# Kernel tuning notes

Hardware: AMD Instinct MI355X
Metric: run time of the kernel (lower is better)

Reference implementation:

```python
import jax, jax.numpy as jnp
import numpy as np

DIM = 4096
N_HEADS = 32
N_KV_HEADS = 8
HEAD_DIM = DIM // N_HEADS  # 128
KV_DIM = N_KV_HEADS * HEAD_DIM  # 1024
B, T = 2, 1024


def setup_inputs() -> dict:
    key = jax.random.key(0)
    ks = jax.random.split(key, 5)
    s1 = 1.0 / np.sqrt(DIM)
    return {
        "x": jax.random.normal(ks[0], (B, T, DIM), dtype=jnp.float32),
        "W1": jax.random.uniform(ks[1], (DIM + 2 * KV_DIM, DIM), dtype=jnp.float32, minval=-s1, maxval=s1),
        "b1": jax.random.uniform(ks[2], (DIM + 2 * KV_DIM,), dtype=jnp.float32, minval=-s1, maxval=s1),
        "W2": jax.random.uniform(ks[3], (DIM, DIM), dtype=jnp.float32, minval=-s1, maxval=s1),
        "b2": jax.random.uniform(ks[4], (DIM,), dtype=jnp.float32, minval=-s1, maxval=s1),
    }


def reference(x, W1, b1, W2, b2):
    Bn, Tn, D = x.shape
    G = N_HEADS // N_KV_HEADS
    qkv = x @ W1.T + b1  # [B,T,D+2*KV_DIM]
    q = qkv[:, :, :DIM]
    k = qkv[:, :, DIM:DIM + KV_DIM]
    v = qkv[:, :, DIM + KV_DIM:]
    # Faithful to torch repeat_interleave(G, dim=-1): scalar-level interleave on flat feature dim
    k = jnp.repeat(k, G, axis=-1)  # [B,T,D]
    v = jnp.repeat(v, G, axis=-1)
    q = q.reshape(Bn, Tn, N_HEADS, HEAD_DIM).transpose(0, 2, 1, 3)  # [B,H,T,hd]
    k = k.reshape(Bn, Tn, N_HEADS, HEAD_DIM).transpose(0, 2, 1, 3)
    v = v.reshape(Bn, Tn, N_HEADS, HEAD_DIM).transpose(0, 2, 1, 3)
    scale = 1.0 / jnp.sqrt(jnp.asarray(HEAD_DIM, dtype=x.dtype))
    qk = jnp.einsum('bhqd,bhkd->bhqk', q, k) * scale  # [B,H,T,T]
    causal = jnp.tril(jnp.ones((Tn, Tn), dtype=bool))
    qk = jnp.where(causal[None, None], qk, jnp.asarray(-jnp.inf, dtype=qk.dtype))
    att = jax.nn.softmax(qk, axis=-1)
    out = jnp.einsum('bhqk,bhkd->bhqd', att, v)  # [B,H,T,hd]
    out = out.transpose(0, 2, 1, 3).reshape(Bn, Tn, D)
    return out @ W2.T + b2
```

## Files before the change

### kernel.cpp

```cpp
#include <hip/hip_runtime.h>

#define DIMX  4096
#define NH    32
#define HD    128
#define BB    2
#define TT    1024
#define MROWS (BB*TT)
#define CQKV  3072
#define SCALE_Q 0.12751743f

typedef _Float16 half_t;
typedef __attribute__((ext_vector_type(4))) _Float16 f16x4;
typedef __attribute__((ext_vector_type(8))) _Float16 f16x8;
typedef __attribute__((ext_vector_type(4))) float    f32x4;

__device__ __forceinline__ void async_copy16(const void* gsrc, void* ldst) {
  __builtin_amdgcn_global_load_lds(
      (const __attribute__((address_space(1))) unsigned int*)gsrc,
      (__attribute__((address_space(3))) unsigned int*)ldst,
      16, 0, 0);
}

__global__ __launch_bounds__(256) void cvt_f32_f16_kernel(
    const float4* __restrict__ src, f16x4* __restrict__ dst, int n4) {
  int stride = gridDim.x * blockDim.x;
  for (int i = blockIdx.x * blockDim.x + threadIdx.x; i < n4; i += stride) {
    float4 f = src[i];
    f16x4 h;
    h.x = (_Float16)f.x; h.y = (_Float16)f.y;
    h.z = (_Float16)f.z; h.w = (_Float16)f.w;
    dst[i] = h;
  }
}

__global__ __launch_bounds__(256) void fold_w1_kernel(
    const float* __restrict__ W1, const float* __restrict__ b1,
    half_t* __restrict__ W1f, float* __restrict__ b1f)
{
  long idx = (long)blockIdx.x * 256 + threadIdx.x;
  int row = (int)(idx >> 10);
  int c4  = ((int)idx & 1023) << 2;
  f16x4 h;
  if (row < 1024) {
    const float* s = W1 + ((long)row << 2) * DIMX + c4;
    float4 a = *(const float4*)s;
    float4 b = *(const float4*)(s + DIMX);
    float4 c = *(const float4*)(s + 2 * DIMX);
    float4 d = *(const float4*)(s + 3 * DIMX);
    h.x = (_Float16)((a.x + b.x + c.x + d.x) * SCALE_Q);
    h.y = (_Float16)((a.y + b.y + c.y + d.y) * SCALE_Q);
    h.z = (_Float16)((a.z + b.z + c.z + d.z) * SCALE_Q);
    h.w = (_Float16)((a.w + b.w + c.w + d.w) * SCALE_Q);
    if (c4 == 0) {
      const float* bb = b1 + ((long)row << 2);
      b1f[row] = (bb[0] + bb[1] + bb[2] + bb[3]) * SCALE_Q;
    }
  } else {
    const float* s = W1 + ((long)(row + 3072)) * DIMX + c4;
    float4 a = *(const float4*)s;
    h.x = (_Float16)a.x; h.y = (_Float16)a.y;
    h.z = (_Float16)a.z; h.w = (_Float16)a.w;
    if (c4 == 0) b1f[row] = b1[row + 3072];
  }
  *(f16x4*)&W1f[(long)row * DIMX + c4] = h;
}

__global__ __launch_bounds__(256) void fold_w2_kernel(
    const float* __restrict__ W2, half_t* __restrict__ W2f)
{
  long idx = (long)blockIdx.x * 256 + threadIdx.x;
  int row = (int)(idx >> 8);
  int j4  = ((int)idx & 255) << 2;
  const float* s = W2 + (long)row * DIMX + ((long)j4 << 2);
  float4 a = *(const float4*)s;
  float4 b = *(const float4*)(s + 4);
  float4 c = *(const float4*)(s + 8);
  float4 d = *(const float4*)(s + 12);
  f16x4 h;
  h.x = (_Float16)(a.x + a.y + a.z + a.w);
  h.y = (_Float16)(b.x + b.y + b.z + b.w);
  h.z = (_Float16)(c.x + c.y + c.z + c.w);
  h.w = (_Float16)(d.x + d.y + d.z + d.w);
  *(f16x4*)&W2f[(long)row * 1024 + j4] = h;
}

template<int OUT_IS_F16>
__global__ __launch_bounds__(256) void gemm_nt_bias(
    const half_t* __restrict__ A, const half_t* __restrict__ Bw,
    const float* __restrict__ bias, void* __restrict__ Cout,
    int M, int N, int K)
{
  __shared__ alignas(16) half_t As[128 * 32];
  __shared__ alignas(16) half_t Bs[128 * 32];

  const int tid  = threadIdx.x;
  const int lane = tid & 63;
  const int w    = tid >> 6;
  const long row0 = (long)blockIdx.y * 128;
  const long col0 = (long)blockIdx.x * 128;

  const int rr = tid >> 2;
  const int cc = (tid & 3) * 8;
  const half_t* ga0 = A  + (row0 + rr)      * K + cc;
  const half_t* ga1 = A  + (row0 + 64 + rr) * K + cc;
  const half_t* gb0 = Bw + (col0 + rr)      * K + cc;
  const half_t* gb1 = Bw + (col0 + 64 + rr) * K + cc;
  half_t* la0 = &As[w * 512];
  half_t* la1 = &As[2048 + w * 512];
  half_t* lb0 = &Bs[w * 512];
  half_t* lb1 = &Bs[2048 + w * 512];

  const int wm = (w >> 1) * 64;
  const int wn = (w & 1) * 64;
  const int fr = lane & 15;
  const int fk = (lane >> 4) * 8;
  const half_t* pa = &As[(wm + fr) * 32 + fk];
  const half_t* pb = &Bs[(wn + fr) * 32 + fk];

  f32x4 acc[4][4] = {};

  for (int kt = 0; kt < K; kt += 32) {
    __syncthreads();
    async_copy16(ga0 + kt, la0);
    async_copy16(ga1 + kt, la1);
    async_copy16(gb0 + kt, lb0);
    async_copy16(gb1 + kt, lb1);
    __syncthreads();

    f16x8 af[4], bf[4];
#pragma unroll
    for (int mi = 0; mi < 4; ++mi) af[mi] = *(const f16x8*)(pa + mi * 16 * 32);
#pragma unroll
    for (int ni = 0; ni < 4; ++ni) bf[ni] = *(const f16x8*)(pb + ni * 16 * 32);
#pragma unroll
    for (int mi = 0; mi < 4; ++mi)
#pragma unroll
      for (int ni = 0; ni < 4; ++ni)
        acc[mi][ni] = __builtin_amdgcn_mfma_f32_16x16x32_f16(
            af[mi], bf[ni], acc[mi][ni], 0, 0, 0);
  }

  const int er = (lane >> 4) * 4;
  const int ec = lane & 15;
#pragma unroll
  for (int mi = 0; mi < 4; ++mi) {
#pragma unroll
    for (int ni = 0; ni < 4; ++ni) {
      long gn = col0 + wn + ni * 16 + ec;
      float bv = bias[gn];
#pragma unroll
      for (int r = 0; r < 4; ++r) {
        long gm = row0 + wm + mi * 16 + er + r;
        float v = acc[mi][ni][r] + bv;
        if (OUT_IS_F16) ((half_t*)Cout)[gm * N + gn] = (half_t)v;
        else            ((float*)Cout)[gm * N + gn]  = v;
      }
    }
  }
}

#define VTS 72
#define PSS 72
__global__ __launch_bounds__(256, 4) void attn_kernel(
    const half_t* __restrict__ qkv,
    half_t* __restrict__ attc)
{
  __shared__ alignas(16) half_t Ks[64 * 32];
  __shared__ alignas(16) half_t Vt[48 * VTS];
  __shared__ alignas(16) half_t Ps[4][16 * PSS];

  const int tid  = threadIdx.x;
  const int lane = tid & 63;
  const int w    = tid >> 6;
  const int low  = lane & 15;
  const int quad = lane >> 4;
  const int bh   = blockIdx.y;
  const int b    = bh >> 5;
  const int h    = bh & 31;
  const long rb  = (long)b * TT;

  if (tid < 8) {
    f16x8 one;
#pragma unroll
    for (int i = 0; i < 8; ++i) one[i] = (_Float16)1.0f;
    *(f16x8*)&Vt[32 * VTS + tid * 8] = one;
  }

  const int srow = tid >> 2;
  const int sc4  = (tid & 3) << 3;
  half_t* ksdst  = &Ks[w * 512];
  half_t* psw    = &Ps[w][0];
  float*  Ob     = (float*)psw;

  for (int pass = 0; pass < 2; ++pass) {
    const int tile = pass ? (int)blockIdx.x : 15 - (int)blockIdx.x;
    const int t0   = tile * 64;
    const int qg   = t0 + 16 * w;

    f16x8 qf = *(const f16x8*)&qkv[(rb + qg + low) * CQKV + h * 32 + quad * 8];

    f32x4 acc0 = {}, acc1 = {}, acc2 = {};
    const f32x4 zero = {};

    for (int c = 0; c <= t0; c += 64) {
      __syncthreads();
      const half_t* kg = &qkv[(rb + c + srow) * CQKV + 1024 + h * 32 + sc4];
      async_copy16(kg, ksdst);
      f16x8 vv = *(const f16x8*)(kg + 1024);
#pragma unroll
      for (int j = 0; j < 8; ++j)
        Vt[(sc4 + j) * VTS + srow] = vv[j];
      __syncthreads();

      f32x4 s[4];
#pragma unroll
      for (int st = 0; st < 4; ++st) {
        f16x8 kf = *(const f16x8*)&Ks[(st * 16 + low) * 32 + quad * 8];
        s[st] = __builtin_amdgcn_mfma_f32_16x16x32_f16(qf, kf, zero, 0, 0, 0);
      }

      const bool diag = (c == t0);
#pragma unroll
      for (int st = 0; st < 4; ++st) {
#pragma unroll
        for (int r = 0; r < 4; ++r) {
          const int key = c + st * 16 + low;
          const int q   = qg + 4 * quad + r;
          float p = __builtin_amdgcn_exp2f(s[st][r]);
          if (diag && key > q) p = 0.f;
          psw[(4 * quad + r) * PSS + st * 16 + low] = (_Float16)p;
        }
      }

      f16x8 p0 = *(const f16x8*)&psw[low * PSS + 0 * 32 + quad * 8];
      f16x8 p1 = *(const f16x8*)&psw[low * PSS + 1 * 32 + quad * 8];

      f16x8 v00 = *(const f16x8*)&Vt[(0  + low) * VTS + 0  + quad * 8];
      f16x8 v01 = *(const f16x8*)&Vt[(0  + low) * VTS + 32 + quad * 8];
      f16x8 v10 = *(const f16x8*)&Vt[(16 + low) * VTS + 0  + quad * 8];
      f16x8 v11 = *(const f16x8*)&Vt[(16 + low) * VTS + 32 + quad * 8];
      f16x8 v20 = *(const f16x8*)&Vt[(32 + low) * VTS + 0  + quad * 8];
      f16x8 v21 = *(const f16x8*)&Vt[(32 + low) * VTS + 32 + quad * 8];

      acc0 = __builtin_amdgcn_mfma_f32_16x16x32_f16(v00, p0, acc0, 0, 0, 0);
      acc0 = __builtin_amdgcn_mfma_f32_16x16x32_f16(v01, p1, acc0, 0, 0, 0);
      acc1 = __builtin_amdgcn_mfma_f32_16x16x32_f16(v10, p0, acc1, 0, 0, 0);
      acc1 = __builtin_amdgcn_mfma_f32_16x16x32_f16(v11, p1, acc1, 0, 0, 0);
      acc2 = __builtin_amdgcn_mfma_f32_16x16x32_f16(v20, p0, acc2, 0, 0, 0);
      acc2 = __builtin_amdgcn_mfma_f32_16x16x32_f16(v21, p1, acc2, 0, 0, 0);
    }

    __syncthreads();

    float linv = 1.0f / __shfl(acc2[0], low);

#pragma unroll
    for (int r = 0; r < 4; ++r) {
      Ob[low * 36 + 0  + 4 * quad + r] = acc0[r] * linv;
      Ob[low * 36 + 16 + 4 * quad + r] = acc1[r] * linv;
    }
    __syncthreads();

    f16x8 ov;
#pragma unroll
    for (int i = 0; i < 8; ++i)
      ov[i] = (_Float16)Ob[low * 36 + quad * 8 + i];
    *(f16x8*)&attc[(rb + qg + low) * 1024 + h * 32 + quad * 8] = ov;
  }
}

extern "C" void kernel_launch(void* const* d_in, const int* in_sizes, int n_in,
                              void* d_out, int out_size, void* d_ws, size_t ws_size,
                              hipStream_t stream) {
  (void)in_sizes; (void)n_in; (void)out_size; (void)ws_size;
  const float* x  = (const float*)d_in[0];
  const float* W1 = (const float*)d_in[1];
  const float* b1 = (const float*)d_in[2];
  const float* W2 = (const float*)d_in[3];
  const float* b2 = (const float*)d_in[4];
  float* out = (float*)d_out;

  const size_t nX   = (size_t)MROWS * DIMX;
  const size_t nW1f = (size_t)CQKV  * DIMX;
  const size_t nW2f = (size_t)DIMX  * 1024;
  const size_t nQKV = (size_t)MROWS * CQKV;
  const size_t nATT = (size_t)MROWS * 1024;

  half_t* ws   = (half_t*)d_ws;
  half_t* xh   = ws;
  half_t* w1f  = xh   + nX;
  half_t* w2f  = w1f  + nW1f;
  half_t* qkvc = w2f  + nW2f;
  half_t* attc = qkvc + nQKV;
  float*  b1f  = (float*)(attc + nATT);

  cvt_f32_f16_kernel<<<4096, 256, 0, stream>>>((const float4*)x, (f16x4*)xh,
                                               (int)(nX / 4));
  fold_w1_kernel<<<12288, 256, 0, stream>>>(W1, b1, w1f, b1f);
  fold_w2_kernel<<<4096, 256, 0, stream>>>(W2, w2f);

  gemm_nt_bias<1><<<dim3(CQKV / 128, MROWS / 128), 256, 0, stream>>>(
      xh, w1f, b1f, (void*)qkvc, MROWS, CQKV, DIMX);

  attn_kernel<<<dim3(8, BB * NH), 256, 0, stream>>>(qkvc, attc);

  gemm_nt_bias<0><<<dim3(DIMX / 128, MROWS / 128), 256, 0, stream>>>(
      attc, w2f, b2, (void*)out, MROWS, DIMX, 1024);
}
```

Measured before the change: 375.7 us.

## Split QKV projection GEMM along K into two partial GEMMs plus reduction

After: 367.8 us. 1.02x faster.

```diff
diff --git a/kernel.cpp b/kernel.cpp
--- a/kernel.cpp
+++ b/kernel.cpp
@@ -159,6 +159,98 @@
   }
 }
 
+__global__ __launch_bounds__(256) void gemm_nt_splitk(
+    const half_t* __restrict__ A, const half_t* __restrict__ Bw,
+    float* __restrict__ Cp0, float* __restrict__ Cp1,
+    int M, int N, int K)
+{
+  __shared__ alignas(16) half_t As[128 * 32];
+  __shared__ alignas(16) half_t Bs[128 * 32];
+
+  const int tid  = threadIdx.x;
+  const int lane = tid & 63;
+  const int w    = tid >> 6;
+  const long row0 = (long)blockIdx.y * 128;
+  const long col0 = (long)blockIdx.x * 128;
+  const int  KH   = K >> 1;
+  const long k0   = (long)blockIdx.z * KH;
+
+  const int rr = tid >> 2;
+  const int cc = (tid & 3) * 8;
+  const half_t* ga0 = A  + (row0 + rr)      * K + k0 + cc;
+  const half_t* ga1 = A  + (row0 + 64 + rr) * K + k0 + cc;
+  const half_t* gb0 = Bw + (col0 + rr)      * K + k0 + cc;
+  const half_t* gb1 = Bw + (col0 + 64 + rr) * K + k0 + cc;
+  half_t* la0 = &As[w * 512];
+  half_t* la1 = &As[2048 + w * 512];
+  half_t* lb0 = &Bs[w * 512];
+  half_t* lb1 = &Bs[2048 + w * 512];
+
+  const int wm = (w >> 1) * 64;
+  const int wn = (w & 1) * 64;
+  const int fr = lane & 15;
+  const int fk = (lane >> 4) * 8;
+  const half_t* pa = &As[(wm + fr) * 32 + fk];
+  const half_t* pb = &Bs[(wn + fr) * 32 + fk];
+
+  f32x4 acc[4][4] = {};
+
+  for (int kt = 0; kt < KH; kt += 32) {
+    __syncthreads();
+    async_copy16(ga0 + kt, la0);
+    async_copy16(ga1 + kt, la1);
+    async_copy16(gb0 + kt, lb0);
+    async_copy16(gb1 + kt, lb1);
+    __syncthreads();
+
+    f16x8 af[4], bf[4];
+#pragma unroll
+    for (int mi = 0; mi < 4; ++mi) af[mi] = *(const f16x8*)(pa + mi * 16 * 32);
+#pragma unroll
+    for (int ni = 0; ni < 4; ++ni) bf[ni] = *(const f16x8*)(pb + ni * 16 * 32);
+#pragma unroll
+    for (int mi = 0; mi < 4; ++mi)
+#pragma unroll
+      for (int ni = 0; ni < 4; ++ni)
+        acc[mi][ni] = __builtin_amdgcn_mfma_f32_16x16x32_f16(
+            af[mi], bf[ni], acc[mi][ni], 0, 0, 0);
+  }
+
+  float* Cp = blockIdx.z ? Cp1 : Cp0;
+  const int er = (lane >> 4) * 4;
+  const int ec = lane & 15;
+#pragma unroll
+  for (int mi = 0; mi < 4; ++mi) {
+#pragma unroll
+    for (int ni = 0; ni < 4; ++ni) {
+      long gn = col0 + wn + ni * 16 + ec;
+#pragma unroll
+      for (int r = 0; r < 4; ++r) {
+        long gm = row0 + wm + mi * 16 + er + r;
+        Cp[gm * N + gn] = acc[mi][ni][r];
+      }
+    }
+  }
+}
+
+__global__ __launch_bounds__(256) void splitk_reduce_kernel(
+    const float4* __restrict__ C0, const float4* __restrict__ C1,
+    const float4* __restrict__ bias4, f16x4* __restrict__ dst)
+{
+  const int col  = blockIdx.x * 256 + threadIdx.x;
+  const long row = blockIdx.y;
+  const long i   = row * (CQKV / 4) + col;
+  float4 a = C0[i];
+  float4 b = C1[i];
+  float4 bv = bias4[col];
+  f16x4 h;
+  h.x = (_Float16)(a.x + b.x + bv.x);
+  h.y = (_Float16)(a.y + b.y + bv.y);
+  h.z = (_Float16)(a.z + b.z + bv.z);
+  h.w = (_Float16)(a.w + b.w + bv.w);
+  dst[i] = h;
+}
+
 #define VTS 72
 #define PSS 72
 __global__ __launch_bounds__(256, 4) void attn_kernel(
@@ -293,14 +385,18 @@
   half_t* qkvc = w2f  + nW2f;
   half_t* attc = qkvc + nQKV;
   float*  b1f  = (float*)(attc + nATT);
+  float*  c1   = (float*)(b1f + 4096);
 
   cvt_f32_f16_kernel<<<4096, 256, 0, stream>>>((const float4*)x, (f16x4*)xh,
                                                (int)(nX / 4));
   fold_w1_kernel<<<12288, 256, 0, stream>>>(W1, b1, w1f, b1f);
   fold_w2_kernel<<<4096, 256, 0, stream>>>(W2, w2f);
 
-  gemm_nt_bias<1><<<dim3(CQKV / 128, MROWS / 128), 256, 0, stream>>>(
-      xh, w1f, b1f, (void*)qkvc, MROWS, CQKV, DIMX);
+  gemm_nt_splitk<<<dim3(CQKV / 128, MROWS / 128, 2), 256, 0, stream>>>(
+      xh, w1f, out , c1 , MROWS, CQKV, DIMX);
+  splitk_reduce_kernel<<<dim3(CQKV / 4 / 256, MROWS), 256, 0, stream>>>(
+      (const float4*)out, (const float4*)c1, (const float4*)b1f,
+      (f16x4*)qkvc);
 
   attn_kernel<<<dim3(8, BB * NH), 256, 0, stream>>>(qkvc, attc);
 
```
